# Kernel tuning notes

Measured on AMD Instinct MI355X. Metric: run time of the kernel, lower is better.

Reference implementation:

```python
import jax, jax.numpy as jnp
import numpy as np

N, F, B = 16384, 512, 4
H = 4          # attn heads
MR = 2         # mlp_ratio
GH = max(F // 4, 32)   # gate hidden = 128
SE = F // 8    # SE bottleneck
FH = 512       # fusion_hidden
E = 3          # num experts
EPS = 1e-5


def setup_inputs() -> dict:
    key = jax.random.key(0)
    ks = jax.random.split(key, 24)
    p = lambda k, s: 0.02 * jax.random.normal(k, s, dtype=jnp.float32)
    return {
        'branches': jax.random.normal(ks[0], (N, F, B), dtype=jnp.float32),
        'conv_pw_w': p(ks[1], (F, F)),          # Conv1d k=1, no bias
        'conv_dw_w': p(ks[2], (F, 3)),          # depthwise k=3
        'gn_w': jnp.ones((F,), jnp.float32), 'gn_b': jnp.zeros((F,), jnp.float32),
        'se_w1': p(ks[3], (SE, F)), 'se_w2': p(ks[4], (F, SE)),
        'ln_attn_w': jnp.ones((F,), jnp.float32), 'ln_attn_b': jnp.zeros((F,), jnp.float32),
        'in_proj_w': p(ks[5], (3 * F, F)), 'in_proj_b': jnp.zeros((3 * F,), jnp.float32),
        'attn_out_w': p(ks[6], (F, F)), 'attn_out_b': jnp.zeros((F,), jnp.float32),
        'ln_ffn_w': jnp.ones((F,), jnp.float32), 'ln_ffn_b': jnp.zeros((F,), jnp.float32),
        'ffn_w1': p(ks[7], (MR * F, F)), 'ffn_b1': jnp.zeros((MR * F,), jnp.float32),
        'ffn_w2': p(ks[8], (F, MR * F)), 'ffn_b2': jnp.zeros((F,), jnp.float32),
        'mlp_ln_w': jnp.ones((F,), jnp.float32), 'mlp_ln_b': jnp.zeros((F,), jnp.float32),
        'mlp_w1': p(ks[9], (MR * F, F)), 'mlp_b1': jnp.zeros((MR * F,), jnp.float32),
        'mlp_w2': p(ks[10], (F, MR * F)), 'mlp_b2': jnp.zeros((F,), jnp.float32),
        'gate_w1': p(ks[11], (GH, 2 * F)), 'gate_b1': jnp.zeros((GH,), jnp.float32),
        'gate_w2': p(ks[12], (E, GH)), 'gate_b2': jnp.zeros((E,), jnp.float32),
        'outp_w': p(ks[13], (FH, F)),
    }


def _ln(x, w, b):
    m = jnp.mean(x, -1, keepdims=True)
    v = jnp.mean((x - m) ** 2, -1, keepdims=True)
    return (x - m) * jax.lax.rsqrt(v + EPS) * w + b


def _gelu(x):
    return jax.nn.gelu(x, approximate=False)


def _forward(branches, conv_pw_w, conv_dw_w, gn_w, gn_b, se_w1, se_w2,
             ln_attn_w, ln_attn_b, in_proj_w, in_proj_b, attn_out_w, attn_out_b,
             ln_ffn_w, ln_ffn_b, ffn_w1, ffn_b1, ffn_w2, ffn_b2,
             mlp_ln_w, mlp_ln_b, mlp_w1, mlp_b1, mlp_w2, mlp_b2,
             gate_w1, gate_b1, gate_w2, gate_b2, outp_w):
    # ---- Conv expert ----
    x1 = jnp.einsum('fg,ngb->nfb', conv_pw_w, branches)          # pointwise conv
    xp = jnp.pad(x1, ((0, 0), (0, 0), (1, 1)))                    # depthwise k=3, pad=1
    w0, w1, w2 = (conv_dw_w[:, k][None, :, None] for k in range(3))
    x1 = w0 * xp[:, :, :-2] + w1 * xp[:, :, 1:-1] + w2 * xp[:, :, 2:]
    s = jnp.mean(x1, -1)                                          # SE squeeze (N,F)
    s = jax.nn.sigmoid(jax.nn.relu(s @ se_w1.T) @ se_w2.T)
    x1 = x1 * s[:, :, None]
    m = jnp.mean(x1, (1, 2), keepdims=True)                       # GroupNorm(1 group)
    v = jnp.mean((x1 - m) ** 2, (1, 2), keepdims=True)
    x1 = (x1 - m) * jax.lax.rsqrt(v + EPS) * gn_w[None, :, None] + gn_b[None, :, None]
    x1 = _gelu(x1)
    # ---- Attention expert (branches as tokens) ----
    t = jnp.swapaxes(branches, 1, 2)                              # (N,B,F)
    h = _ln(t, ln_attn_w, ln_attn_b)
    qkv = h @ in_proj_w.T + in_proj_b
    q, k, vv = jnp.split(qkv, 3, axis=-1)
    dh = F // H
    q = q.reshape(N, B, H, dh) * (dh ** -0.5)
    k = k.reshape(N, B, H, dh)
    vv = vv.reshape(N, B, H, dh)
    att = jax.nn.softmax(jnp.einsum('nqhd,nkhd->nhqk', q, k), axis=-1)
    ao = jnp.einsum('nhqk,nkhd->nqhd', att, vv).reshape(N, B, F)
    t = t + ao @ attn_out_w.T + attn_out_b
    h = _ln(t, ln_ffn_w, ln_ffn_b)
    t = t + _gelu(h @ ffn_w1.T + ffn_b1) @ ffn_w2.T + ffn_b2
    x2 = jnp.swapaxes(t, 1, 2)
    # ---- MLP expert ----
    t3 = jnp.swapaxes(branches, 1, 2)
    h3 = _ln(t3, mlp_ln_w, mlp_ln_b)
    t3 = t3 + _gelu(h3 @ mlp_w1.T + mlp_b1) @ mlp_w2.T + mlp_b2
    x3 = jnp.swapaxes(t3, 1, 2)
    # ---- Gating ----
    ctx = jnp.concatenate([jnp.mean(branches, -1), jnp.max(branches, -1)], axis=-1)
    logits = _gelu(ctx @ gate_w1.T + gate_b1) @ gate_w2.T + gate_b2
    alpha = jax.nn.softmax(logits, axis=-1)                       # (N,3)
    fused = (alpha[:, 0, None, None] * x1 + alpha[:, 1, None, None] * x2
             + alpha[:, 2, None, None] * x3)
    return jnp.einsum('of,nfb->nob', outp_w, fused)               # out_proj k=1 conv


def reference(branches, conv_pw_w, conv_dw_w, gn_w, gn_b, se_w1, se_w2,
              ln_attn_w, ln_attn_b, in_proj_w, in_proj_b, attn_out_w, attn_out_b,
              ln_ffn_w, ln_ffn_b, ffn_w1, ffn_b1, ffn_w2, ffn_b2,
              mlp_ln_w, mlp_ln_b, mlp_w1, mlp_b1, mlp_w2, mlp_b2,
              gate_w1, gate_b1, gate_w2, gate_b2, outp_w):
    return _forward(branches, conv_pw_w, conv_dw_w, gn_w, gn_b, se_w1, se_w2,
                    ln_attn_w, ln_attn_b, in_proj_w, in_proj_b, attn_out_w, attn_out_b,
                    ln_ffn_w, ln_ffn_b, ffn_w1, ffn_b1, ffn_w2, ffn_b2,
                    mlp_ln_w, mlp_ln_b, mlp_w1, mlp_b1, mlp_w2, mlp_b2,
                    gate_w1, gate_b1, gate_w2, gate_b2, outp_w)
```

## Files before the change

kernel.cpp:

```cpp
#include <hip/hip_runtime.h>
#include <math.h>


#define N_TOT 16384
#define EPSV 1e-5f

typedef unsigned short u16;
typedef unsigned int   u32;
typedef __attribute__((ext_vector_type(8))) short  short8;
typedef __attribute__((ext_vector_type(4))) float  floatx4;

__device__ __forceinline__ float gelu_exact(float x) {
    return 0.5f * x * (1.0f + erff(x * 0.70710678118654752440f));
}
__device__ __forceinline__ float wave_sum(float v) {
    #pragma unroll
    for (int o = 32; o > 0; o >>= 1) v += __shfl_xor(v, o);
    return v;
}
__device__ __forceinline__ u16 f2bf(float f) {
    u32 u = __float_as_uint(f);
    return (u16)((u + 0x7fffu + ((u >> 16) & 1u)) >> 16);
}
__device__ __forceinline__ u32 pack2(float lo, float hi) {
    return (u32)f2bf(lo) | ((u32)f2bf(hi) << 16);
}
__device__ __forceinline__ float bf1f(u16 u) { return __uint_as_float((u32)u << 16); }
__device__ __forceinline__ float2 bf2f2(u32 u) {
    return make_float2(__uint_as_float(u << 16), __uint_as_float(u & 0xffff0000u));
}
__device__ __forceinline__ void gload_lds16(const void* g, void* l) {
    __builtin_amdgcn_global_load_lds(
        (const __attribute__((address_space(1))) unsigned int*)g,
        (__attribute__((address_space(3))) unsigned int*)l, 16, 0, 0);
}

#define BARR() asm volatile("s_barrier" ::: "memory")
#define VMW(N) asm volatile("s_waitcnt vmcnt(" #N ")" ::: "memory")

#define W_CONVPW 0
#define W_INPROJ 262144
#define W_ATTNO  1048576
#define W_FFN1   1310720
#define W_FFN2   1835008
#define W_MLP1   2359296
#define W_MLP2   2883584
#define W_GATE1  3407872
#define W_SE1    3538944
#define W_SE2    3571712
#define W_OUTP   3604480
#define W_TOT    3866624

__global__ __launch_bounds__(256) void k_w2b(
        const float* __restrict__ p0, const float* __restrict__ p1,
        const float* __restrict__ p2, const float* __restrict__ p3,
        const float* __restrict__ p4, const float* __restrict__ p5,
        const float* __restrict__ p6, const float* __restrict__ p7,
        const float* __restrict__ p8, const float* __restrict__ p9,
        const float* __restrict__ p10, u16* __restrict__ dst)
{
    int i = blockIdx.x * 256 + threadIdx.x;
    if (i >= W_TOT) return;
    const float* s; int off;
    if      (i < W_INPROJ) { s = p0;  off = W_CONVPW; }
    else if (i < W_ATTNO)  { s = p1;  off = W_INPROJ; }
    else if (i < W_FFN1)   { s = p2;  off = W_ATTNO; }
    else if (i < W_FFN2)   { s = p3;  off = W_FFN1; }
    else if (i < W_MLP1)   { s = p4;  off = W_FFN2; }
    else if (i < W_MLP2)   { s = p5;  off = W_MLP1; }
    else if (i < W_GATE1)  { s = p6;  off = W_MLP2; }
    else if (i < W_SE1)    { s = p7;  off = W_GATE1; }
    else if (i < W_SE2)    { s = p8;  off = W_SE1; }
    else if (i < W_OUTP)   { s = p9;  off = W_SE2; }
    else                   { s = p10; off = W_OUTP; }
    dst[i] = f2bf(s[i - off]);
}

__global__ __launch_bounds__(256) void k_prep_ln(const float* __restrict__ br,
        int baseN, u16* __restrict__ Tb, u16* __restrict__ CTX,
        const float* __restrict__ law, const float* __restrict__ lab, u16* __restrict__ LNA,
        const float* __restrict__ lmw, const float* __restrict__ lmb, u16* __restrict__ LNM)
{
    __shared__ float lds[4][4][516];
    int t = threadIdx.x;
    int s0 = blockIdx.x * 4;
    #pragma unroll
    for (int s = 0; s < 4; ++s) {
        const float* p = br + (size_t)(baseN + s0 + s) * 2048;
        u16* c = CTX + (size_t)(s0 + s) * 1024;
        #pragma unroll
        for (int i = 0; i < 2; ++i) {
            int f = t + i * 256;
            float4 v = *(const float4*)(p + f * 4);
            lds[s][0][f] = v.x; lds[s][1][f] = v.y; lds[s][2][f] = v.z; lds[s][3][f] = v.w;
            c[f]       = f2bf((v.x + v.y + v.z + v.w) * 0.25f);
            c[512 + f] = f2bf(fmaxf(fmaxf(v.x, v.y), fmaxf(v.z, v.w)));
        }
    }
    __syncthreads();
    int wv = t >> 6, lane = t & 63, f0 = lane * 8;
    #pragma unroll
    for (int p4i = 0; p4i < 4; ++p4i) {
        int idx = wv * 4 + p4i;
        int s = idx >> 2, b = idx & 3;
        float xv[8];
        #pragma unroll
        for (int i = 0; i < 8; ++i) xv[i] = lds[s][b][f0 + i];
        float sm = 0.f;
        #pragma unroll
        for (int i = 0; i < 8; ++i) sm += xv[i];
        sm = wave_sum(sm);
        float m = sm * (1.f / 512.f);
        float q = 0.f;
        #pragma unroll
        for (int i = 0; i < 8; ++i) { float d = xv[i] - m; q += d * d; }
        q = wave_sum(q);
        float rs = rsqrtf(q * (1.f / 512.f) + EPSV);
        size_t row = (size_t)(s0 + s) * 4 + b;
        *(uint4*)(Tb + row * 512 + f0) = make_uint4(pack2(xv[0], xv[1]), pack2(xv[2], xv[3]),
                                                    pack2(xv[4], xv[5]), pack2(xv[6], xv[7]));
        float o[8];
        #pragma unroll
        for (int i = 0; i < 8; ++i) o[i] = (xv[i] - m) * rs * law[f0 + i] + lab[f0 + i];
        *(uint4*)(LNA + row * 512 + f0) = make_uint4(pack2(o[0], o[1]), pack2(o[2], o[3]),
                                                     pack2(o[4], o[5]), pack2(o[6], o[7]));
        #pragma unroll
        for (int i = 0; i < 8; ++i) o[i] = (xv[i] - m) * rs * lmw[f0 + i] + lmb[f0 + i];
        *(uint4*)(LNM + row * 512 + f0) = make_uint4(pack2(o[0], o[1]), pack2(o[2], o[3]),
                                                     pack2(o[4], o[5]), pack2(o[6], o[7]));
    }
}

__global__ __launch_bounds__(256) void k_ln_b(const u16* __restrict__ X,
        const float* __restrict__ w, const float* __restrict__ b, u16* __restrict__ O)
{
    int t = threadIdx.x;
    int wave = t >> 6, lane = t & 63;
    size_t r = (size_t)blockIdx.x * 4 + wave;
    int f0 = lane * 8;
    uint4 raw = *(const uint4*)(X + r * 512 + f0);
    float xv[8];
    { float2 a = bf2f2(raw.x); xv[0] = a.x; xv[1] = a.y; }
    { float2 a = bf2f2(raw.y); xv[2] = a.x; xv[3] = a.y; }
    { float2 a = bf2f2(raw.z); xv[4] = a.x; xv[5] = a.y; }
    { float2 a = bf2f2(raw.w); xv[6] = a.x; xv[7] = a.y; }
    float s = 0.f;
    #pragma unroll
    for (int i = 0; i < 8; ++i) s += xv[i];
    s = wave_sum(s);
    float m = s * (1.f / 512.f);
    float q = 0.f;
    #pragma unroll
    for (int i = 0; i < 8; ++i) { float d = xv[i] - m; q += d * d; }
    q = wave_sum(q);
    float rs = rsqrtf(q * (1.f / 512.f) + EPSV);
    float o[8];
    #pragma unroll
    for (int i = 0; i < 8; ++i) o[i] = (xv[i] - m) * rs * w[f0 + i] + b[f0 + i];
    *(uint4*)(O + r * 512 + f0) = make_uint4(pack2(o[0], o[1]), pack2(o[2], o[3]),
                                             pack2(o[4], o[5]), pack2(o[6], o[7]));
}


#define STAGE(SLOT, TILE) do {                                                \
    const u16* sm_ = ((SLOT) < 2) ? A : W;                                    \
    int rb_ = (((SLOT) < 2) ? m0 : n0) + ((SLOT) & 1) * 128;                  \
    int k0_ = (TILE) * 64;                                                    \
    u16* db_ = lds + (((TILE) & 1) * 32768) + (SLOT) * 8192;                  \
    _Pragma("unroll")                                                         \
    for (int l_ = 0; l_ < 2; ++l_) {                                          \
        int L_ = (l_ * 512 + tid) * 16;                                       \
        int row_ = L_ >> 7;                                                   \
        int ir_ = (L_ & 127) ^ ((row_ & 7) << 4);                             \
        gload_lds16(sm_ + (size_t)(rb_ + row_) * K + k0_ + (ir_ >> 1),        \
                    db_ + (L_ >> 1));                                         \
    } } while (0)

#define QUAD(MH, NH, STAGESTMT) do {                                          \
    const u16* lb_ = lds + cur * 32768;                                       \
    short8 a_[4][2], b_[2][2];                                                \
    _Pragma("unroll")                                                         \
    for (int mi = 0; mi < 4; ++mi)                                            \
        _Pragma("unroll")                                                     \
        for (int ks = 0; ks < 2; ++ks)                                        \
            a_[mi][ks] = *(const short8*)(lb_ + (MH) * 8192 + arow[mi] + gcol[ks]); \
    _Pragma("unroll")                                                         \
    for (int ni = 0; ni < 2; ++ni)                                            \
        _Pragma("unroll")                                                     \
        for (int ks = 0; ks < 2; ++ks)                                        \
            b_[ni][ks] = *(const short8*)(lb_ + 16384 + (NH) * 8192 + brow[ni] + gcol[ks]); \
    STAGESTMT;                                                                \
    BARR();                                                                   \
    __builtin_amdgcn_s_setprio(1);                                            \
    _Pragma("unroll")                                                         \
    for (int ks = 0; ks < 2; ++ks)                                            \
        _Pragma("unroll")                                                     \
        for (int mi = 0; mi < 4; ++mi)                                        \
            _Pragma("unroll")                                                 \
            for (int ni = 0; ni < 2; ++ni)                                    \
                acc[MH][NH][mi][ni] = __builtin_amdgcn_mfma_f32_16x16x32_bf16( \
                    a_[mi][ks], b_[ni][ks], acc[MH][NH][mi][ni], 0, 0, 0);    \
    __builtin_amdgcn_s_setprio(0);                                            \
} while (0)

template<int EPI, bool HAS_BIAS, bool HAS_RES, int STORE>
__global__ __launch_bounds__(512, 2) void k_gemm256(
        const u16* __restrict__ A, const u16* __restrict__ W,
        const float* __restrict__ bias, const u16* __restrict__ Res,
        void* __restrict__ Cout, int Ncols, int K, int baseN, int nTX,
        const float* __restrict__ dwp, u16* __restrict__ Sout)
{
    __shared__ __align__(16) u16 lds[65536];
    const int tid = threadIdx.x;
    const int wid = tid >> 6, lane = tid & 63;
    const int lr = lane & 15, kg = lane >> 4;
    const int wm = (wid >> 2) * 64;
    const int wn = (wid & 3) * 32;

    int nwg = gridDim.x, orig = blockIdx.x;
    int q = nwg >> 3, r = nwg & 7;
    int xcd = orig & 7, lin = orig >> 3;
    int wgid = (xcd < r ? xcd * (q + 1) : r * (q + 1) + (xcd - r) * q) + lin;
    const int m0 = (wgid / nTX) * 256, n0 = (wgid % nTX) * 256;

    int arow[4], brow[2], gcol[2];
    #pragma unroll
    for (int mi = 0; mi < 4; ++mi) arow[mi] = (wm + mi * 16 + lr) * 64;
    #pragma unroll
    for (int ni = 0; ni < 2; ++ni) brow[ni] = (wn + ni * 16 + lr) * 64;
    #pragma unroll
    for (int ks = 0; ks < 2; ++ks) gcol[ks] = (ks * 32 + kg * 8) ^ ((lr & 7) << 3);

    floatx4 acc[2][2][4][2] = {};

    STAGE(0, 0); STAGE(2, 0); STAGE(1, 0); STAGE(3, 0);

    const int NT = K >> 6;
    int cur = 0;
    for (int t = 0; t < NT - 1; ++t) {
        int nx = t + 1;
        VMW(4); BARR(); QUAD(0, 0, STAGE(0, nx));
        VMW(4); BARR(); QUAD(1, 0, STAGE(2, nx));
        VMW(4); BARR(); QUAD(0, 1, STAGE(1, nx));
                BARR(); QUAD(1, 1, STAGE(3, nx));
        cur ^= 1;
    }
    VMW(4); BARR(); QUAD(0, 0, (void)0);
    VMW(2); BARR(); QUAD(1, 0, (void)0);
    VMW(0); BARR(); QUAD(0, 1, (void)0);
            BARR(); QUAD(1, 1, (void)0);

    int rm = kg * 4;
    #pragma unroll
    for (int MH = 0; MH < 2; ++MH)
    #pragma unroll
    for (int NH = 0; NH < 2; ++NH)
    #pragma unroll
    for (int ni = 0; ni < 2; ++ni) {
        int n = n0 + NH * 128 + wn + ni * 16 + lr;
        float bv = HAS_BIAS ? bias[n] : 0.f;
        float w0, w1, w2;
        if (STORE == 3) { w0 = dwp[n * 3]; w1 = dwp[n * 3 + 1]; w2 = dwp[n * 3 + 2]; }
        #pragma unroll
        for (int mi = 0; mi < 4; ++mi) {
            int mb = m0 + MH * 128 + wm + mi * 16 + rm;
            float vv[4];
            #pragma unroll
            for (int rr = 0; rr < 4; ++rr) {
                float v = acc[MH][NH][mi][ni][rr] + bv;
                if (EPI == 1) v = gelu_exact(v);
                else if (EPI == 2) v = fmaxf(v, 0.f);
                else if (EPI == 3) v = 1.f / (1.f + expf(-v));
                vv[rr] = v;
            }
            if (STORE == 2) {
                *(float4*)((float*)Cout + (size_t)(baseN + (mb >> 2)) * 2048 + (size_t)n * 4)
                    = make_float4(vv[0], vv[1], vv[2], vv[3]);
            } else if (STORE == 3) {
                float y0 = w1 * vv[0] + w2 * vv[1];
                float y1 = w0 * vv[0] + w1 * vv[1] + w2 * vv[2];
                float y2 = w0 * vv[1] + w1 * vv[2] + w2 * vv[3];
                float y3 = w0 * vv[2] + w1 * vv[3];
                u16* xp = (u16*)Cout + (size_t)mb * Ncols + n;
                xp[0] = f2bf(y0);
                xp[Ncols] = f2bf(y1);
                xp[2 * Ncols] = f2bf(y2);
                xp[3 * Ncols] = f2bf(y3);
                Sout[(size_t)(mb >> 2) * Ncols + n] = f2bf((y0 + y1 + y2 + y3) * 0.25f);
            } else {
                #pragma unroll
                for (int rr = 0; rr < 4; ++rr) {
                    float v = vv[rr];
                    if (HAS_RES) v += bf1f(Res[(size_t)(mb + rr) * Ncols + n]);
                    ((u16*)Cout)[(size_t)(mb + rr) * Ncols + n] = f2bf(v);
                }
            }
        }
    }
}

template<int EPI, bool HAS_BIAS, bool HAS_RES, int STORE>
__global__ __launch_bounds__(256) void k_mfma_gemm(
        const u16* __restrict__ A, const u16* __restrict__ W,
        const float* __restrict__ bias, const u16* __restrict__ Res,
        void* __restrict__ Cout, int M, int Ncols, int K, int baseN)
{
    __shared__ u16 As[128 * 32];
    __shared__ u16 Bs[128 * 32];
    int t = threadIdx.x;
    int wid = t >> 6, lane = t & 63;
    int wm = (wid >> 1) * 64, wn = (wid & 1) * 64;
    int m0 = blockIdx.y * 128, n0 = blockIdx.x * 128;
    int srow = t >> 2;
    int scol = (((t & 3) ^ ((srow >> 1) & 3)) * 8);
    int aR0 = min(m0 + srow, M - 1),      aR1 = min(m0 + 64 + srow, M - 1);
    int bR0 = min(n0 + srow, Ncols - 1),  bR1 = min(n0 + 64 + srow, Ncols - 1);
    const u16* Ap0 = A + (size_t)aR0 * K + scol;
    const u16* Ap1 = A + (size_t)aR1 * K + scol;
    const u16* Wp0 = W + (size_t)bR0 * K + scol;
    const u16* Wp1 = W + (size_t)bR1 * K + scol;
    u16* AsT0 = As + t * 8;  u16* AsT1 = As + 2048 + t * 8;
    u16* BsT0 = Bs + t * 8;  u16* BsT1 = Bs + 2048 + t * 8;

    int kg = lane >> 4, lr = lane & 15;
    int cb = kg ^ ((lr >> 1) & 3);
    const u16* aF = As + (wm + lr) * 32 + cb * 8;
    const u16* bF = Bs + (wn + lr) * 32 + cb * 8;

    floatx4 acc[4][4] = {};
    for (int k0 = 0; k0 < K; k0 += 32) {
        __syncthreads();
        gload_lds16(Ap0 + k0, AsT0);
        gload_lds16(Ap1 + k0, AsT1);
        gload_lds16(Wp0 + k0, BsT0);
        gload_lds16(Wp1 + k0, BsT1);
        __syncthreads();
        short8 a[4], b[4];
        #pragma unroll
        for (int i = 0; i < 4; ++i) {
            a[i] = *(const short8*)(aF + i * 512);
            b[i] = *(const short8*)(bF + i * 512);
        }
        #pragma unroll
        for (int i = 0; i < 4; ++i)
            #pragma unroll
            for (int j = 0; j < 4; ++j)
                acc[i][j] = __builtin_amdgcn_mfma_f32_16x16x32_bf16(a[i], b[j], acc[i][j], 0, 0, 0);
    }
    int rm = (lane >> 4) * 4;
    #pragma unroll
    for (int j = 0; j < 4; ++j) {
        int n = n0 + wn + j * 16 + lr;
        float bv = HAS_BIAS ? bias[min(n, Ncols - 1)] : 0.f;
        #pragma unroll
        for (int i = 0; i < 4; ++i) {
            int mb = m0 + wm + i * 16 + rm;
            float vv[4];
            #pragma unroll
            for (int r = 0; r < 4; ++r) {
                float v = acc[i][j][r] + bv;
                if (EPI == 1) v = gelu_exact(v);
                else if (EPI == 2) v = fmaxf(v, 0.f);
                else if (EPI == 3) v = 1.f / (1.f + expf(-v));
                vv[r] = v;
            }
            #pragma unroll
            for (int r = 0; r < 4; ++r) {
                int m = mb + r;
                if (m < M && n < Ncols) {
                    float v = vv[r];
                    if (HAS_RES) v += bf1f(Res[(size_t)m * Ncols + n]);
                    if (STORE == 0) ((float*)Cout)[(size_t)m * Ncols + n] = v;
                    else            ((u16*)Cout)[(size_t)m * Ncols + n] = f2bf(v);
                }
            }
        }
    }
// ... 66 lines not shown
        float dx = xr[b].x - m, dy = xr[b].y - m;
        q += dx * dx + dy * dy;
    }
    q = wave_sum(q);
    if (lane == 0) red[4 + wave] = q;
    __syncthreads();
    float rs = rsqrtf((red[4] + red[5] + red[6] + red[7]) * (1.f / 2048.f) + EPSV);
    const float* a = alpha + (size_t)(baseN + ls) * 3;
    float a0 = a[0], a1 = a[1], a2 = a[2];
    float gw0 = gnw[f], gw1 = gnw[f + 1], gb0 = gnb[f], gb1 = gnb[f + 1];
    #pragma unroll
    for (int b = 0; b < 4; ++b) {
        float x1a = gelu_exact((xr[b].x - m) * rs * gw0 + gb0);
        float x1b = gelu_exact((xr[b].y - m) * rs * gw1 + gb1);
        float2 v2 = bf2f2(*(const u32*)(X2 + (ls * 4 + b) * 512 + f));
        float2 v3 = bf2f2(*(const u32*)(X3 + (ls * 4 + b) * 512 + f));
        *(u32*)(FU + (ls * 4 + b) * 512 + f) =
            pack2(a0 * x1a + a1 * v2.x + a2 * v3.x,
                  a0 * x1b + a1 * v2.y + a2 * v3.y);
    }
}

__global__ __launch_bounds__(256) void k_gate2(const u16* __restrict__ G1,
        const float* __restrict__ w2, const float* __restrict__ b2,
        float* __restrict__ alpha, int CH)
{
    int s = blockIdx.x * 256 + threadIdx.x;
    if (s >= CH) return;
    float l0 = b2[0], l1 = b2[1], l2 = b2[2];
    const u16* g = G1 + (size_t)s * 128;
    for (int j = 0; j < 128; j += 2) {
        float2 gg = bf2f2(*(const u32*)(g + j));
        l0 += gg.x * w2[j]       + gg.y * w2[j + 1];
        l1 += gg.x * w2[128 + j] + gg.y * w2[129 + j];
        l2 += gg.x * w2[256 + j] + gg.y * w2[257 + j];
    }
    float mx = fmaxf(l0, fmaxf(l1, l2));
    float e0 = expf(l0 - mx), e1 = expf(l1 - mx), e2 = expf(l2 - mx);
    float inv = 1.f / (e0 + e1 + e2);
    float* a = alpha + (size_t)s * 3;
    a[0] = e0 * inv; a[1] = e1 * inv; a[2] = e2 * inv;
}

extern "C" void kernel_launch(void* const* d_in, const int* in_sizes, int n_in,
                              void* d_out, int out_size, void* d_ws, size_t ws_size,
                              hipStream_t stream)
{
    (void)in_sizes; (void)n_in; (void)out_size;
    const float* br         = (const float*)d_in[0];
    const float* conv_pw_w  = (const float*)d_in[1];
    const float* conv_dw_w  = (const float*)d_in[2];
    const float* gn_w       = (const float*)d_in[3];
    const float* gn_b       = (const float*)d_in[4];
    const float* se_w1      = (const float*)d_in[5];
    const float* se_w2      = (const float*)d_in[6];
    const float* ln_attn_w  = (const float*)d_in[7];
    const float* ln_attn_b  = (const float*)d_in[8];
    const float* in_proj_w  = (const float*)d_in[9];
    const float* in_proj_b  = (const float*)d_in[10];
    const float* attn_out_w = (const float*)d_in[11];
    const float* attn_out_b = (const float*)d_in[12];
    const float* ln_ffn_w   = (const float*)d_in[13];
    const float* ln_ffn_b   = (const float*)d_in[14];
    const float* ffn_w1     = (const float*)d_in[15];
    const float* ffn_b1     = (const float*)d_in[16];
    const float* ffn_w2     = (const float*)d_in[17];
    const float* ffn_b2     = (const float*)d_in[18];
    const float* mlp_ln_w   = (const float*)d_in[19];
    const float* mlp_ln_b   = (const float*)d_in[20];
    const float* mlp_w1     = (const float*)d_in[21];
    const float* mlp_b1     = (const float*)d_in[22];
    const float* mlp_w2     = (const float*)d_in[23];
    const float* mlp_b2     = (const float*)d_in[24];
    const float* gate_w1    = (const float*)d_in[25];
    const float* gate_b1    = (const float*)d_in[26];
    const float* gate_w2    = (const float*)d_in[27];
    const float* gate_b2    = (const float*)d_in[28];
    const float* outp_w     = (const float*)d_in[29];
    float* out = (float*)d_out;

    char* ws = (char*)d_ws;
    float* alpha = (float*)ws;
    u16* Wb = (u16*)(ws + 196608);
    const size_t CB = 196608 + (size_t)W_TOT * 2;
    int CH = N_TOT;
    while (CH > 64 && CB + (size_t)CH * 31104ULL > ws_size) CH >>= 1;

    char* p = ws + CB;
    u16* Tb   = (u16*)p; p += (size_t)CH * 4096;
    char* CTXS = p;      p += (size_t)CH * 2048;
    u16* LNA  = (u16*)p; p += (size_t)CH * 4096;
    u16* LNM  = (u16*)p; p += (size_t)CH * 4096;
    u16* QKV  = (u16*)p; p += (size_t)CH * 12288;
    u16* AOXP = (u16*)p; p += (size_t)CH * 4096;
    u16* H1   = (u16*)p; p += (size_t)CH * 128;
    u16* G1   = (u16*)p; p += (size_t)CH * 256;
    u16* CTX  = (u16*)CTXS;
    u16* S    = (u16*)CTXS;
    u16* SIGb = (u16*)(CTXS + (size_t)CH * 1024);
    u16* U    = QKV;
    u16* LNF  = LNA;
    u16* FU   = LNM;

    u16* O16 = (u16*)d_out;

    k_w2b<<<(W_TOT + 255) / 256, 256, 0, stream>>>(
        conv_pw_w, in_proj_w, attn_out_w, ffn_w1, ffn_w2, mlp_w1, mlp_w2,
        gate_w1, se_w1, se_w2, outp_w, Wb);

    const int Ri = CH * 4;
    auto g128 = [](int M, int Nc) { return dim3((Nc + 127) / 128, (M + 127) / 128); };
    auto g256 = [](int M, int Nc) { return dim3((M / 256) * (Nc / 256)); };

    for (int c0 = 0; c0 < N_TOT; c0 += CH) {
        u16* X2b  = O16 + (size_t)c0 * 2048;
        u16* T2X3 = O16 + (size_t)N_TOT * 2048 + (size_t)c0 * 2048;

        k_prep_ln<<<CH / 4, 256, 0, stream>>>(br, c0, Tb, CTX,
                                              ln_attn_w, ln_attn_b, LNA,
                                              mlp_ln_w, mlp_ln_b, LNM);
        k_mfma_gemm<1, true, false, 1><<<g128(CH, 128), 256, 0, stream>>>(
            CTX, Wb + W_GATE1, gate_b1, nullptr, G1, CH, 128, 1024, 0);
        k_gate2<<<(CH + 255) / 256, 256, 0, stream>>>(G1, gate_w2, gate_b2,
                                                      alpha + (size_t)c0 * 3, CH);
        k_gemm256<0, true, false, 1><<<g256(Ri, 1536), 512, 0, stream>>>(
            LNA, Wb + W_INPROJ, in_proj_b, nullptr, QKV, 1536, 512, 0, 6, nullptr, nullptr);
        k_attn<<<CH, 256, 0, stream>>>(QKV, AOXP);
        k_gemm256<0, true, true, 1><<<g256(Ri, 512), 512, 0, stream>>>(
            AOXP, Wb + W_ATTNO, attn_out_b, Tb, T2X3, 512, 512, 0, 2, nullptr, nullptr);
        k_ln_b<<<Ri / 4, 256, 0, stream>>>(T2X3, ln_ffn_w, ln_ffn_b, LNF);
        k_gemm256<1, true, false, 1><<<g256(Ri, 1024), 512, 0, stream>>>(
            LNF, Wb + W_FFN1, ffn_b1, nullptr, U, 1024, 512, 0, 4, nullptr, nullptr);
        k_gemm256<0, true, true, 1><<<g256(Ri, 512), 512, 0, stream>>>(
            U, Wb + W_FFN2, ffn_b2, T2X3, X2b, 512, 1024, 0, 2, nullptr, nullptr);
        k_gemm256<1, true, false, 1><<<g256(Ri, 1024), 512, 0, stream>>>(
            LNM, Wb + W_MLP1, mlp_b1, nullptr, U, 1024, 512, 0, 4, nullptr, nullptr);
        k_gemm256<0, true, true, 1><<<g256(Ri, 512), 512, 0, stream>>>(
            U, Wb + W_MLP2, mlp_b2, Tb, T2X3, 512, 1024, 0, 2, nullptr, nullptr);
        k_gemm256<0, false, false, 3><<<g256(Ri, 512), 512, 0, stream>>>(
            Tb, Wb + W_CONVPW, nullptr, nullptr, AOXP, 512, 512, 0, 2, conv_dw_w, S);
        k_mfma_gemm<2, false, false, 1><<<g128(CH, 64), 256, 0, stream>>>(
            S, Wb + W_SE1, nullptr, nullptr, H1, CH, 64, 512, 0);
        k_mfma_gemm<3, false, false, 1><<<g128(CH, 512), 256, 0, stream>>>(
            H1, Wb + W_SE2, nullptr, nullptr, SIGb, CH, 512, 64, 0);
        k_gnfin_fuse<<<CH, 256, 0, stream>>>(AOXP, SIGb, gn_w, gn_b,
                                             X2b, T2X3, alpha, c0, FU);
        k_gemm256<0, false, false, 2><<<g256(Ri, 512), 512, 0, stream>>>(
            FU, Wb + W_OUTP, nullptr, nullptr, out, 512, 512, c0, 2, nullptr, nullptr);
    }
}
```

Measured before the change: 1.036 ms.

## Stage bf16 GEMM epilogue through swizzled LDS for coalesced 16-byte stores

For the plain bf16-store GEMM variant, the MFMA operands are swapped so each lane holds four consecutive output columns. Bias and residual can then be loaded as vectors, and results are packed into an XOR-swizzled LDS tile. The whole 256x256 tile is then written to global memory with coalesced 16-byte stores, replacing scattered 2-byte per-element stores and residual loads. This adds an extra barrier and an LDS round trip at the end of each tile.

After: 1.163 ms. 12.2% more time.

```diff
diff --git a/kernel.cpp b/kernel.cpp
--- a/kernel.cpp
+++ b/kernel.cpp
@@ -34,9 +34,15 @@
         (const __attribute__((address_space(1))) unsigned int*)g,
         (__attribute__((address_space(3))) unsigned int*)l, 16, 0, 0);
 }
+template<bool S>
+__device__ __forceinline__ floatx4 mfma_do(short8 a, short8 b, floatx4 c) {
+    if (S) return __builtin_amdgcn_mfma_f32_16x16x32_bf16(b, a, c, 0, 0, 0);
+    else   return __builtin_amdgcn_mfma_f32_16x16x32_bf16(a, b, c, 0, 0, 0);
+}
 
 #define BARR() asm volatile("s_barrier" ::: "memory")
 #define VMW(N) asm volatile("s_waitcnt vmcnt(" #N ")" ::: "memory")
+#define LGKM0() asm volatile("s_waitcnt lgkmcnt(0)" ::: "memory")
 
 #define W_CONVPW 0
 #define W_INPROJ 262144
@@ -198,8 +204,8 @@
         for (int mi = 0; mi < 4; ++mi)                                        \
             _Pragma("unroll")                                                 \
             for (int ni = 0; ni < 2; ++ni)                                    \
-                acc[MH][NH][mi][ni] = __builtin_amdgcn_mfma_f32_16x16x32_bf16( \
-                    a_[mi][ks], b_[ni][ks], acc[MH][NH][mi][ni], 0, 0, 0);    \
+                acc[MH][NH][mi][ni] = mfma_do<SWAPD>(                         \
+                    a_[mi][ks], b_[ni][ks], acc[MH][NH][mi][ni]);             \
     __builtin_amdgcn_s_setprio(0);                                            \
 } while (0)
 
@@ -210,6 +216,7 @@
         void* __restrict__ Cout, int Ncols, int K, int baseN, int nTX,
         const float* __restrict__ dwp, u16* __restrict__ Sout)
 {
+    constexpr bool SWAPD = (STORE == 1);
     __shared__ __align__(16) u16 lds[65536];
     const int tid = threadIdx.x;
     const int wid = tid >> 6, lane = tid & 63;
@@ -250,49 +257,85 @@
     VMW(0); BARR(); QUAD(0, 1, (void)0);
             BARR(); QUAD(1, 1, (void)0);
 
-    int rm = kg * 4;
-    #pragma unroll
-    for (int MH = 0; MH < 2; ++MH)
-    #pragma unroll
-    for (int NH = 0; NH < 2; ++NH)
-    #pragma unroll
-    for (int ni = 0; ni < 2; ++ni) {
-        int n = n0 + NH * 128 + wn + ni * 16 + lr;
-        float bv = HAS_BIAS ? bias[n] : 0.f;
-        float w0, w1, w2;
-        if (STORE == 3) { w0 = dwp[n * 3]; w1 = dwp[n * 3 + 1]; w2 = dwp[n * 3 + 2]; }
-        #pragma unroll
-        for (int mi = 0; mi < 4; ++mi) {
-            int mb = m0 + MH * 128 + wm + mi * 16 + rm;
-            float vv[4];
+    if (STORE == 1) {
+        BARR();
+        #pragma unroll
+        for (int MH = 0; MH < 2; ++MH)
+        #pragma unroll
+        for (int NH = 0; NH < 2; ++NH)
+        #pragma unroll
+        for (int ni = 0; ni < 2; ++ni) {
+            int nl = NH * 128 + wn + ni * 16 + kg * 4;
+            float4 bv4 = HAS_BIAS ? *(const float4*)(bias + n0 + nl)
+                                  : make_float4(0.f, 0.f, 0.f, 0.f);
             #pragma unroll
-            for (int rr = 0; rr < 4; ++rr) {
-                float v = acc[MH][NH][mi][ni][rr] + bv;
-                if (EPI == 1) v = gelu_exact(v);
-                else if (EPI == 2) v = fmaxf(v, 0.f);
-                else if (EPI == 3) v = 1.f / (1.f + expf(-v));
-                vv[rr] = v;
-            }
-            if (STORE == 2) {
-                *(float4*)((float*)Cout + (size_t)(baseN + (mb >> 2)) * 2048 + (size_t)n * 4)
-                    = make_float4(vv[0], vv[1], vv[2], vv[3]);
-            } else if (STORE == 3) {
-                float y0 = w1 * vv[0] + w2 * vv[1];
-                float y1 = w0 * vv[0] + w1 * vv[1] + w2 * vv[2];
-                float y2 = w0 * vv[1] + w1 * vv[2] + w2 * vv[3];
-                float y3 = w0 * vv[2] + w1 * vv[3];
-                u16* xp = (u16*)Cout + (size_t)mb * Ncols + n;
-                xp[0] = f2bf(y0);
-                xp[Ncols] = f2bf(y1);
-                xp[2 * Ncols] = f2bf(y2);
-                xp[3 * Ncols] = f2bf(y3);
-                Sout[(size_t)(mb >> 2) * Ncols + n] = f2bf((y0 + y1 + y2 + y3) * 0.25f);
-            } else {
+            for (int mi = 0; mi < 4; ++mi) {
+                int ml = MH * 128 + wm + mi * 16 + lr;
+                float v[4];
                 #pragma unroll
                 for (int rr = 0; rr < 4; ++rr) {
-                    float v = vv[rr];
-                    if (HAS_RES) v += bf1f(Res[(size_t)(mb + rr) * Ncols + n]);
-                    ((u16*)Cout)[(size_t)(mb + rr) * Ncols + n] = f2bf(v);
+                    float x = acc[MH][NH][mi][ni][rr] + (&bv4.x)[rr];
+                    if (EPI == 1) x = gelu_exact(x);
+                    else if (EPI == 2) x = fmaxf(x, 0.f);
+                    else if (EPI == 3) x = 1.f / (1.f + expf(-x));
+                    v[rr] = x;
+                }
+                if (HAS_RES) {
+                    uint2 r8 = *(const uint2*)(Res + (size_t)(m0 + ml) * Ncols + n0 + nl);
+                    float2 ra = bf2f2(r8.x), rb = bf2f2(r8.y);
+                    v[0] += ra.x; v[1] += ra.y; v[2] += rb.x; v[3] += rb.y;
+                }
+                int byte = ml * 512 + ((nl * 2) ^ ((ml & 7) << 4));
+                *(uint2*)((char*)lds + byte) = make_uint2(pack2(v[0], v[1]), pack2(v[2], v[3]));
+            }
+        }
+        LGKM0();
+        BARR();
+        #pragma unroll
+        for (int i = 0; i < 16; ++i) {
+            int L = tid * 256 + i * 16;
+            int ml = L >> 9, off = L & 511;
+            uint4 d = *(const uint4*)((const char*)lds + ml * 512 + (off ^ ((ml & 7) << 4)));
+            *(uint4*)((u16*)Cout + (size_t)(m0 + ml) * Ncols + n0 + (off >> 1)) = d;
+        }
+    } else {
+        int rm = kg * 4;
+        #pragma unroll
+        for (int MH = 0; MH < 2; ++MH)
+        #pragma unroll
+        for (int NH = 0; NH < 2; ++NH)
+        #pragma unroll
+        for (int ni = 0; ni < 2; ++ni) {
+            int n = n0 + NH * 128 + wn + ni * 16 + lr;
+            float bv = HAS_BIAS ? bias[n] : 0.f;
+            float w0, w1, w2;
+            if (STORE == 3) { w0 = dwp[n * 3]; w1 = dwp[n * 3 + 1]; w2 = dwp[n * 3 + 2]; }
+            #pragma unroll
+            for (int mi = 0; mi < 4; ++mi) {
+                int mb = m0 + MH * 128 + wm + mi * 16 + rm;
+                float vv[4];
+                #pragma unroll
+                for (int rr = 0; rr < 4; ++rr) {
+                    float v = acc[MH][NH][mi][ni][rr] + bv;
+                    if (EPI == 1) v = gelu_exact(v);
+                    else if (EPI == 2) v = fmaxf(v, 0.f);
+                    else if (EPI == 3) v = 1.f / (1.f + expf(-v));
+                    vv[rr] = v;
+                }
+                if (STORE == 2) {
+                    *(float4*)((float*)Cout + (size_t)(baseN + (mb >> 2)) * 2048 + (size_t)n * 4)
+                        = make_float4(vv[0], vv[1], vv[2], vv[3]);
+                } else if (STORE == 3) {
+                    float y0 = w1 * vv[0] + w2 * vv[1];
+                    float y1 = w0 * vv[0] + w1 * vv[1] + w2 * vv[2];
+                    float y2 = w0 * vv[1] + w1 * vv[2] + w2 * vv[3];
+                    float y3 = w0 * vv[2] + w1 * vv[3];
+                    u16* xp = (u16*)Cout + (size_t)mb * Ncols + n;
+                    xp[0] = f2bf(y0);
+                    xp[Ncols] = f2bf(y1);
+                    xp[2 * Ncols] = f2bf(y2);
+                    xp[3 * Ncols] = f2bf(y3);
+                    Sout[(size_t)(mb >> 2) * Ncols + n] = f2bf((y0 + y1 + y2 + y3) * 0.25f);
                 }
             }
         }
```

## Restructure bf16 GEMM mainloop to 4-slot K=32 pipeline with larger per-wave tiles

Applied to the files above, without the earlier changes.

The 256x256 GEMM mainloop now uses K tiles of 32 instead of 64, held in a 4-slot LDS ring with three tiles in flight, replacing the two-buffer quadrant schedule. Each wave now owns a 128x64 output region (8x4 MFMA accumulators) rather than four 64x32 quadrants. Each tile is computed in two MFMA half-steps, with the A and B staging loads for a later tile issued between them. The aim is deeper load/compute overlap and more fragment reuse per LDS read. In exchange there are more barriers per K element and the same accumulator register count under the 512x2 launch bounds.

Result: slower. 1.349 ms (+30.2%).

```diff
diff --git a/kernel.cpp b/kernel.cpp
--- a/kernel.cpp
+++ b/kernel.cpp
@@ -162,44 +162,58 @@
 }
 
 
-#define STAGE(SLOT, TILE) do {                                                \
-    const u16* sm_ = ((SLOT) < 2) ? A : W;                                    \
-    int rb_ = (((SLOT) < 2) ? m0 : n0) + ((SLOT) & 1) * 128;                  \
-    int k0_ = (TILE) * 64;                                                    \
-    u16* db_ = lds + (((TILE) & 1) * 32768) + (SLOT) * 8192;                  \
+#define STG_A(TILE) do {                                                      \
+    int sl_ = (TILE) & 3;                                                     \
     _Pragma("unroll")                                                         \
     for (int l_ = 0; l_ < 2; ++l_) {                                          \
-        int L_ = (l_ * 512 + tid) * 16;                                       \
-        int row_ = L_ >> 7;                                                   \
-        int ir_ = (L_ & 127) ^ ((row_ & 7) << 4);                             \
-        gload_lds16(sm_ + (size_t)(rb_ + row_) * K + k0_ + (ir_ >> 1),        \
-                    db_ + (L_ >> 1));                                         \
+        int E_ = (l_ * 512 + tid) * 8;                                        \
+        int r_ = E_ >> 6, c_ = E_ & 63;                                       \
+        int cp_ = c_ ^ ((r_ & 7) << 3);                                       \
+        gload_lds16(A + (size_t)(m0 + r_ + ((cp_ >> 5) << 7)) * K             \
+                        + (TILE) * 32 + (cp_ & 31),                           \
+                    lds + sl_ * 16384 + E_);                                  \
     } } while (0)
 
-#define QUAD(MH, NH, STAGESTMT) do {                                          \
-    const u16* lb_ = lds + cur * 32768;                                       \
-    short8 a_[4][2], b_[2][2];                                                \
+#define STG_B(TILE) do {                                                      \
+    int sl_ = (TILE) & 3;                                                     \
+    _Pragma("unroll")                                                         \
+    for (int l_ = 0; l_ < 2; ++l_) {                                          \
+        int E_ = (l_ * 512 + tid) * 8;                                        \
+        int r_ = E_ >> 6, c_ = E_ & 63;                                       \
+        int cp_ = c_ ^ ((r_ & 7) << 3);                                       \
+        gload_lds16(W + (size_t)(n0 + r_ + ((cp_ >> 5) << 7)) * K             \
+                        + (TILE) * 32 + (cp_ & 31),                           \
+                    lds + sl_ * 16384 + 8192 + E_);                           \
+    } } while (0)
+
+#define TILE_BODY(S, SA, SB) do {                                             \
+    const u16* lb_ = lds + (S) * 16384;                                       \
+    short8 a_[4], b_[4];                                                      \
+    _Pragma("unroll")                                                         \
+    for (int ni = 0; ni < 4; ++ni) b_[ni] = *(const short8*)(lb_ + 8192 + boff[ni]); \
+    _Pragma("unroll")                                                         \
+    for (int mi = 0; mi < 4; ++mi) a_[mi] = *(const short8*)(lb_ + aoff[mi]); \
+    SA;                                                                       \
+    BARR();                                                                   \
+    __builtin_amdgcn_s_setprio(1);                                            \
     _Pragma("unroll")                                                         \
     for (int mi = 0; mi < 4; ++mi)                                            \
         _Pragma("unroll")                                                     \
-        for (int ks = 0; ks < 2; ++ks)                                        \
-            a_[mi][ks] = *(const short8*)(lb_ + (MH) * 8192 + arow[mi] + gcol[ks]); \
+        for (int ni = 0; ni < 4; ++ni)                                        \
+            acc[mi][ni] = __builtin_amdgcn_mfma_f32_16x16x32_bf16(            \
+                a_[mi], b_[ni], acc[mi][ni], 0, 0, 0);                        \
+    __builtin_amdgcn_s_setprio(0);                                            \
     _Pragma("unroll")                                                         \
-    for (int ni = 0; ni < 2; ++ni)                                            \
-        _Pragma("unroll")                                                     \
-        for (int ks = 0; ks < 2; ++ks)                                        \
-            b_[ni][ks] = *(const short8*)(lb_ + 16384 + (NH) * 8192 + brow[ni] + gcol[ks]); \
-    STAGESTMT;                                                                \
+    for (int mi = 0; mi < 4; ++mi) a_[mi] = *(const short8*)(lb_ + aoff[4 + mi]); \
+    SB;                                                                       \
     BARR();                                                                   \
     __builtin_amdgcn_s_setprio(1);                                            \
     _Pragma("unroll")                                                         \
-    for (int ks = 0; ks < 2; ++ks)                                            \
+    for (int mi = 0; mi < 4; ++mi)                                            \
         _Pragma("unroll")                                                     \
-        for (int mi = 0; mi < 4; ++mi)                                        \
-            _Pragma("unroll")                                                 \
-            for (int ni = 0; ni < 2; ++ni)                                    \
-                acc[MH][NH][mi][ni] = __builtin_amdgcn_mfma_f32_16x16x32_bf16( \
-                    a_[mi][ks], b_[ni][ks], acc[MH][NH][mi][ni], 0, 0, 0);    \
+        for (int ni = 0; ni < 4; ++ni)                                        \
+            acc[4 + mi][ni] = __builtin_amdgcn_mfma_f32_16x16x32_bf16(        \
+                a_[mi], b_[ni], acc[4 + mi][ni], 0, 0, 0);                    \
     __builtin_amdgcn_s_setprio(0);                                            \
 } while (0)
 
@@ -214,8 +228,8 @@
     const int tid = threadIdx.x;
     const int wid = tid >> 6, lane = tid & 63;
     const int lr = lane & 15, kg = lane >> 4;
-    const int wm = (wid >> 2) * 64;
-    const int wn = (wid & 3) * 32;
+    const int wm = (wid >> 2) * 128;
+    const int wn = (wid & 3) * 64;
 
     int nwg = gridDim.x, orig = blockIdx.x;
     int q = nwg >> 3, r = nwg & 7;
@@ -223,51 +237,48 @@
     int wgid = (xcd < r ? xcd * (q + 1) : r * (q + 1) + (xcd - r) * q) + lin;
     const int m0 = (wgid / nTX) * 256, n0 = (wgid % nTX) * 256;
 
-    int arow[4], brow[2], gcol[2];
-    #pragma unroll
-    for (int mi = 0; mi < 4; ++mi) arow[mi] = (wm + mi * 16 + lr) * 64;
-    #pragma unroll
-    for (int ni = 0; ni < 2; ++ni) brow[ni] = (wn + ni * 16 + lr) * 64;
-    #pragma unroll
-    for (int ks = 0; ks < 2; ++ks) gcol[ks] = (ks * 32 + kg * 8) ^ ((lr & 7) << 3);
-
-    floatx4 acc[2][2][4][2] = {};
-
-    STAGE(0, 0); STAGE(2, 0); STAGE(1, 0); STAGE(3, 0);
-
-    const int NT = K >> 6;
-    int cur = 0;
-    for (int t = 0; t < NT - 1; ++t) {
-        int nx = t + 1;
-        VMW(4); BARR(); QUAD(0, 0, STAGE(0, nx));
-        VMW(4); BARR(); QUAD(1, 0, STAGE(2, nx));
-        VMW(4); BARR(); QUAD(0, 1, STAGE(1, nx));
-                BARR(); QUAD(1, 1, STAGE(3, nx));
-        cur ^= 1;
-    }
-    VMW(4); BARR(); QUAD(0, 0, (void)0);
-    VMW(2); BARR(); QUAD(1, 0, (void)0);
-    VMW(0); BARR(); QUAD(0, 1, (void)0);
-            BARR(); QUAD(1, 1, (void)0);
-
-    int rm = kg * 4;
-    #pragma unroll
-    for (int MH = 0; MH < 2; ++MH)
-    #pragma unroll
-    for (int NH = 0; NH < 2; ++NH)
-    #pragma unroll
-    for (int ni = 0; ni < 2; ++ni) {
-        int n = n0 + NH * 128 + wn + ni * 16 + lr;
+    int aoff[8], boff[4];
+    #pragma unroll
+    for (int mi = 0; mi < 8; ++mi) {
+        int R = wm + mi * 16 + lr;
+        int rr_ = R & 127;
+        aoff[mi] = rr_ * 64 + ((((R >> 7) << 5) + kg * 8) ^ ((rr_ & 7) << 3));
+    }
+    #pragma unroll
+    for (int ni = 0; ni < 4; ++ni) {
+        int R = wn + ni * 16 + lr;
+        int rr_ = R & 127;
+        boff[ni] = rr_ * 64 + ((((R >> 7) << 5) + kg * 8) ^ ((rr_ & 7) << 3));
+    }
+
+    floatx4 acc[8][4] = {};
+
+    STG_A(0); STG_B(0);
+    STG_A(1); STG_B(1);
+    STG_A(2); STG_B(2);
+
+    const int NT = K >> 5;
+    for (int t = 0; t < NT - 3; ++t) {
+        VMW(8); BARR();
+        TILE_BODY(t & 3, STG_A(t + 3), STG_B(t + 3));
+    }
+    VMW(8); BARR(); TILE_BODY((NT - 3) & 3, (void)0, (void)0);
+    VMW(4); BARR(); TILE_BODY((NT - 2) & 3, (void)0, (void)0);
+    VMW(0); BARR(); TILE_BODY((NT - 1) & 3, (void)0, (void)0);
+
+    #pragma unroll
+    for (int ni = 0; ni < 4; ++ni) {
+        int n = n0 + wn + ni * 16 + lr;
         float bv = HAS_BIAS ? bias[n] : 0.f;
         float w0, w1, w2;
         if (STORE == 3) { w0 = dwp[n * 3]; w1 = dwp[n * 3 + 1]; w2 = dwp[n * 3 + 2]; }
         #pragma unroll
-        for (int mi = 0; mi < 4; ++mi) {
-            int mb = m0 + MH * 128 + wm + mi * 16 + rm;
+        for (int mi = 0; mi < 8; ++mi) {
+            int mb = m0 + wm + mi * 16 + kg * 4;
             float vv[4];
             #pragma unroll
             for (int rr = 0; rr < 4; ++rr) {
-                float v = acc[MH][NH][mi][ni][rr] + bv;
+                float v = acc[mi][ni][rr] + bv;
                 if (EPI == 1) v = gelu_exact(v);
                 else if (EPI == 2) v = fmaxf(v, 0.f);
                 else if (EPI == 3) v = 1.f / (1.f + expf(-v));
```

## Fold LayerNorm affine into following GEMM weights and epilogue

Applied to the files above, without the earlier changes.

Folds the LayerNorm weight into the in_proj, ffn1 and mlp1 weight rows, and precomputes per-column sums and bias constants once per call. The GEMMs then read the raw bf16 activations and apply per-row mean/rstd in the epilogue. This removes writing and reading the normalized LNA, LNM and LNF tensors and turns the ffn LayerNorm kernel into a stats-only pass. The cost is more epilogue work per element and a numerical change, since the mean is now subtracted after a bf16 GEMM on uncentered inputs.

Result: slower. 1.057 ms (+2.0%).

```diff
diff --git a/kernel.cpp b/kernel.cpp
--- a/kernel.cpp
+++ b/kernel.cpp
@@ -76,10 +76,50 @@
     dst[i] = f2bf(s[i - off]);
 }
 
+__global__ __launch_bounds__(256) void k_wfold(
+        const float* __restrict__ wA, const float* __restrict__ lnwA,
+        const float* __restrict__ lnbA, const float* __restrict__ biasA,
+        const float* __restrict__ wF, const float* __restrict__ lnwF,
+        const float* __restrict__ lnbF, const float* __restrict__ biasF,
+        const float* __restrict__ wM, const float* __restrict__ lnwM,
+        const float* __restrict__ lnbM, const float* __restrict__ biasM,
+        u16* __restrict__ Wb,
+        float* __restrict__ sA, float* __restrict__ cA,
+        float* __restrict__ sF, float* __restrict__ cF,
+        float* __restrict__ sM, float* __restrict__ cM)
+{
+    __shared__ float rs_[4], rc_[4];
+    int r = blockIdx.x, t = threadIdx.x;
+    const float *W, *lnw, *lnb, *bias;
+    u16* dst; float *sp, *cp; int row;
+    if (r < 1536)      { W = wA; lnw = lnwA; lnb = lnbA; bias = biasA;
+                         dst = Wb + W_INPROJ; sp = sA; cp = cA; row = r; }
+    else if (r < 2560) { W = wF; lnw = lnwF; lnb = lnbF; bias = biasF;
+                         dst = Wb + W_FFN1;   sp = sF; cp = cF; row = r - 1536; }
+    else               { W = wM; lnw = lnwM; lnb = lnbM; bias = biasM;
+                         dst = Wb + W_MLP1;   sp = sM; cp = cM; row = r - 2560; }
+    const float* wr = W + (size_t)row * 512;
+    float s = 0.f, c = 0.f;
+    #pragma unroll
+    for (int i = 0; i < 2; ++i) {
+        int k = t + i * 256;
+        float wv = lnw[k] * wr[k];
+        dst[(size_t)row * 512 + k] = f2bf(wv);
+        s += wv;
+        c += lnb[k] * wr[k];
+    }
+    s = wave_sum(s); c = wave_sum(c);
+    if ((t & 63) == 0) { rs_[t >> 6] = s; rc_[t >> 6] = c; }
+    __syncthreads();
+    if (t == 0) {
+        sp[row] = rs_[0] + rs_[1] + rs_[2] + rs_[3];
+        cp[row] = rc_[0] + rc_[1] + rc_[2] + rc_[3] + bias[row];
+    }
+}
+
 __global__ __launch_bounds__(256) void k_prep_ln(const float* __restrict__ br,
         int baseN, u16* __restrict__ Tb, u16* __restrict__ CTX,
-        const float* __restrict__ law, const float* __restrict__ lab, u16* __restrict__ LNA,
-        const float* __restrict__ lmw, const float* __restrict__ lmb, u16* __restrict__ LNM)
+        float2* __restrict__ STA)
 {
     __shared__ float lds[4][4][516];
     int t = threadIdx.x;
@@ -119,20 +159,12 @@
         size_t row = (size_t)(s0 + s) * 4 + b;
         *(uint4*)(Tb + row * 512 + f0) = make_uint4(pack2(xv[0], xv[1]), pack2(xv[2], xv[3]),
                                                     pack2(xv[4], xv[5]), pack2(xv[6], xv[7]));
-        float o[8];
-        #pragma unroll
-        for (int i = 0; i < 8; ++i) o[i] = (xv[i] - m) * rs * law[f0 + i] + lab[f0 + i];
-        *(uint4*)(LNA + row * 512 + f0) = make_uint4(pack2(o[0], o[1]), pack2(o[2], o[3]),
-                                                     pack2(o[4], o[5]), pack2(o[6], o[7]));
-        #pragma unroll
-        for (int i = 0; i < 8; ++i) o[i] = (xv[i] - m) * rs * lmw[f0 + i] + lmb[f0 + i];
-        *(uint4*)(LNM + row * 512 + f0) = make_uint4(pack2(o[0], o[1]), pack2(o[2], o[3]),
-                                                     pack2(o[4], o[5]), pack2(o[6], o[7]));
-    }
-}
-
-__global__ __launch_bounds__(256) void k_ln_b(const u16* __restrict__ X,
-        const float* __restrict__ w, const float* __restrict__ b, u16* __restrict__ O)
+        if (lane == 0) STA[row] = make_float2(rs, rs * m);
+    }
+}
+
+__global__ __launch_bounds__(256) void k_lnstats(const u16* __restrict__ X,
+        float2* __restrict__ ST)
 {
     int t = threadIdx.x;
     int wave = t >> 6, lane = t & 63;
@@ -154,11 +186,7 @@
     for (int i = 0; i < 8; ++i) { float d = xv[i] - m; q += d * d; }
     q = wave_sum(q);
     float rs = rsqrtf(q * (1.f / 512.f) + EPSV);
-    float o[8];
-    #pragma unroll
-    for (int i = 0; i < 8; ++i) o[i] = (xv[i] - m) * rs * w[f0 + i] + b[f0 + i];
-    *(uint4*)(O + r * 512 + f0) = make_uint4(pack2(o[0], o[1]), pack2(o[2], o[3]),
-                                             pack2(o[4], o[5]), pack2(o[6], o[7]));
+    if (lane == 0) ST[r] = make_float2(rs, rs * m);
 }
 
 
@@ -203,12 +231,14 @@
     __builtin_amdgcn_s_setprio(0);                                            \
 } while (0)
 
-template<int EPI, bool HAS_BIAS, bool HAS_RES, int STORE>
+template<int EPI, bool HAS_BIAS, bool HAS_RES, int STORE, bool LNFOLD>
 __global__ __launch_bounds__(512, 2) void k_gemm256(
         const u16* __restrict__ A, const u16* __restrict__ W,
         const float* __restrict__ bias, const u16* __restrict__ Res,
         void* __restrict__ Cout, int Ncols, int K, int baseN, int nTX,
-        const float* __restrict__ dwp, u16* __restrict__ Sout)
+        const float* __restrict__ dwp, u16* __restrict__ Sout,
+        const float2* __restrict__ Astat, const float* __restrict__ Scol,
+        const float* __restrict__ Ccol)
 {
     __shared__ __align__(16) u16 lds[65536];
     const int tid = threadIdx.x;
@@ -259,6 +289,8 @@
     for (int ni = 0; ni < 2; ++ni) {
         int n = n0 + NH * 128 + wn + ni * 16 + lr;
         float bv = HAS_BIAS ? bias[n] : 0.f;
+        float s_n = 0.f, c_n = 0.f;
+        if (LNFOLD) { s_n = Scol[n]; c_n = Ccol[n]; }
         float w0, w1, w2;
         if (STORE == 3) { w0 = dwp[n * 3]; w1 = dwp[n * 3 + 1]; w2 = dwp[n * 3 + 2]; }
         #pragma unroll
@@ -267,7 +299,13 @@
             float vv[4];
             #pragma unroll
             for (int rr = 0; rr < 4; ++rr) {
-                float v = acc[MH][NH][mi][ni][rr] + bv;
+                float v;
+                if (LNFOLD) {
+                    float2 st = Astat[mb + rr];
+                    v = acc[MH][NH][mi][ni][rr] * st.x - st.y * s_n + c_n;
+                } else {
+                    v = acc[MH][NH][mi][ni][rr] + bv;
+                }
                 if (EPI == 1) v = gelu_exact(v);
                 else if (EPI == 2) v = fmaxf(v, 0.f);
                 else if (EPI == 3) v = 1.f / (1.f + expf(-v));
@@ -525,31 +563,41 @@
     char* ws = (char*)d_ws;
     float* alpha = (float*)ws;
     u16* Wb = (u16*)(ws + 196608);
-    const size_t CB = 196608 + (size_t)W_TOT * 2;
+    float* sA = (float*)(ws + 196608 + (size_t)W_TOT * 2);
+    float* cA = sA + 1536;
+    float* sF = cA + 1536;
+    float* cF = sF + 1024;
+    float* sM = cF + 1024;
+    float* cM = sM + 1024;
+    const size_t CB = 196608 + (size_t)W_TOT * 2 + 28672;
     int CH = N_TOT;
-    while (CH > 64 && CB + (size_t)CH * 31104ULL > ws_size) CH >>= 1;
+    while (CH > 64 && CB + (size_t)CH * 27072ULL > ws_size) CH >>= 1;
 
     char* p = ws + CB;
-    u16* Tb   = (u16*)p; p += (size_t)CH * 4096;
-    char* CTXS = p;      p += (size_t)CH * 2048;
-    u16* LNA  = (u16*)p; p += (size_t)CH * 4096;
-    u16* LNM  = (u16*)p; p += (size_t)CH * 4096;
-    u16* QKV  = (u16*)p; p += (size_t)CH * 12288;
-    u16* AOXP = (u16*)p; p += (size_t)CH * 4096;
-    u16* H1   = (u16*)p; p += (size_t)CH * 128;
-    u16* G1   = (u16*)p; p += (size_t)CH * 256;
+    u16* Tb    = (u16*)p;    p += (size_t)CH * 4096;
+    char* CTXS = p;          p += (size_t)CH * 2048;
+    u16* FU    = (u16*)p;    p += (size_t)CH * 4096;
+    u16* QKV   = (u16*)p;    p += (size_t)CH * 12288;
+    u16* AOXP  = (u16*)p;    p += (size_t)CH * 4096;
+    u16* H1    = (u16*)p;    p += (size_t)CH * 128;
+    u16* G1    = (u16*)p;    p += (size_t)CH * 256;
+    float2* STA = (float2*)p; p += (size_t)CH * 32;
+    float2* ST2 = (float2*)p; p += (size_t)CH * 32;
     u16* CTX  = (u16*)CTXS;
     u16* S    = (u16*)CTXS;
     u16* SIGb = (u16*)(CTXS + (size_t)CH * 1024);
     u16* U    = QKV;
-    u16* LNF  = LNA;
-    u16* FU   = LNM;
 
     u16* O16 = (u16*)d_out;
 
     k_w2b<<<(W_TOT + 255) / 256, 256, 0, stream>>>(
         conv_pw_w, in_proj_w, attn_out_w, ffn_w1, ffn_w2, mlp_w1, mlp_w2,
         gate_w1, se_w1, se_w2, outp_w, Wb);
+    k_wfold<<<3584, 256, 0, stream>>>(
+        in_proj_w, ln_attn_w, ln_attn_b, in_proj_b,
+        ffn_w1, ln_ffn_w, ln_ffn_b, ffn_b1,
+        mlp_w1, mlp_ln_w, mlp_ln_b, mlp_b1,
+        Wb, sA, cA, sF, cF, sM, cM);
 
     const int Ri = CH * 4;
     auto g128 = [](int M, int Nc) { return dim3((Nc + 127) / 128, (M + 127) / 128); };
@@ -559,36 +607,42 @@
         u16* X2b  = O16 + (size_t)c0 * 2048;
         u16* T2X3 = O16 + (size_t)N_TOT * 2048 + (size_t)c0 * 2048;
 
-        k_prep_ln<<<CH / 4, 256, 0, stream>>>(br, c0, Tb, CTX,
-                                              ln_attn_w, ln_attn_b, LNA,
-                                              mlp_ln_w, mlp_ln_b, LNM);
+        k_prep_ln<<<CH / 4, 256, 0, stream>>>(br, c0, Tb, CTX, STA);
         k_mfma_gemm<1, true, false, 1><<<g128(CH, 128), 256, 0, stream>>>(
             CTX, Wb + W_GATE1, gate_b1, nullptr, G1, CH, 128, 1024, 0);
         k_gate2<<<(CH + 255) / 256, 256, 0, stream>>>(G1, gate_w2, gate_b2,
                                                       alpha + (size_t)c0 * 3, CH);
-        k_gemm256<0, true, false, 1><<<g256(Ri, 1536), 512, 0, stream>>>(
-            LNA, Wb + W_INPROJ, in_proj_b, nullptr, QKV, 1536, 512, 0, 6, nullptr, nullptr);
+        k_gemm256<0, false, false, 1, true><<<g256(Ri, 1536), 512, 0, stream>>>(
+            Tb, Wb + W_INPROJ, nullptr, nullptr, QKV, 1536, 512, 0, 6,
+            nullptr, nullptr, STA, sA, cA);
         k_attn<<<CH, 256, 0, stream>>>(QKV, AOXP);
-        k_gemm256<0, true, true, 1><<<g256(Ri, 512), 512, 0, stream>>>(
-            AOXP, Wb + W_ATTNO, attn_out_b, Tb, T2X3, 512, 512, 0, 2, nullptr, nullptr);
-        k_ln_b<<<Ri / 4, 256, 0, stream>>>(T2X3, ln_ffn_w, ln_ffn_b, LNF);
-        k_gemm256<1, true, false, 1><<<g256(Ri, 1024), 512, 0, stream>>>(
-            LNF, Wb + W_FFN1, ffn_b1, nullptr, U, 1024, 512, 0, 4, nullptr, nullptr);
-        k_gemm256<0, true, true, 1><<<g256(Ri, 512), 512, 0, stream>>>(
-            U, Wb + W_FFN2, ffn_b2, T2X3, X2b, 512, 1024, 0, 2, nullptr, nullptr);
-        k_gemm256<1, true, false, 1><<<g256(Ri, 1024), 512, 0, stream>>>(
-            LNM, Wb + W_MLP1, mlp_b1, nullptr, U, 1024, 512, 0, 4, nullptr, nullptr);
-        k_gemm256<0, true, true, 1><<<g256(Ri, 512), 512, 0, stream>>>(
-            U, Wb + W_MLP2, mlp_b2, Tb, T2X3, 512, 1024, 0, 2, nullptr, nullptr);
-        k_gemm256<0, false, false, 3><<<g256(Ri, 512), 512, 0, stream>>>(
-            Tb, Wb + W_CONVPW, nullptr, nullptr, AOXP, 512, 512, 0, 2, conv_dw_w, S);
+        k_gemm256<0, true, true, 1, false><<<g256(Ri, 512), 512, 0, stream>>>(
+            AOXP, Wb + W_ATTNO, attn_out_b, Tb, T2X3, 512, 512, 0, 2,
+            nullptr, nullptr, nullptr, nullptr, nullptr);
+        k_lnstats<<<Ri / 4, 256, 0, stream>>>(T2X3, ST2);
+        k_gemm256<1, false, false, 1, true><<<g256(Ri, 1024), 512, 0, stream>>>(
+            T2X3, Wb + W_FFN1, nullptr, nullptr, U, 1024, 512, 0, 4,
+            nullptr, nullptr, ST2, sF, cF);
+        k_gemm256<0, true, true, 1, false><<<g256(Ri, 512), 512, 0, stream>>>(
+            U, Wb + W_FFN2, ffn_b2, T2X3, X2b, 512, 1024, 0, 2,
+            nullptr, nullptr, nullptr, nullptr, nullptr);
+        k_gemm256<1, false, false, 1, true><<<g256(Ri, 1024), 512, 0, stream>>>(
+            Tb, Wb + W_MLP1, nullptr, nullptr, U, 1024, 512, 0, 4,
+            nullptr, nullptr, STA, sM, cM);
+        k_gemm256<0, true, true, 1, false><<<g256(Ri, 512), 512, 0, stream>>>(
+            U, Wb + W_MLP2, mlp_b2, Tb, T2X3, 512, 1024, 0, 2,
+            nullptr, nullptr, nullptr, nullptr, nullptr);
+        k_gemm256<0, false, false, 3, false><<<g256(Ri, 512), 512, 0, stream>>>(
+            Tb, Wb + W_CONVPW, nullptr, nullptr, AOXP, 512, 512, 0, 2,
+            conv_dw_w, S, nullptr, nullptr, nullptr);
         k_mfma_gemm<2, false, false, 1><<<g128(CH, 64), 256, 0, stream>>>(
             S, Wb + W_SE1, nullptr, nullptr, H1, CH, 64, 512, 0);
         k_mfma_gemm<3, false, false, 1><<<g128(CH, 512), 256, 0, stream>>>(
             H1, Wb + W_SE2, nullptr, nullptr, SIGb, CH, 512, 64, 0);
         k_gnfin_fuse<<<CH, 256, 0, stream>>>(AOXP, SIGb, gn_w, gn_b,
                                              X2b, T2X3, alpha, c0, FU);
-        k_gemm256<0, false, false, 2><<<g256(Ri, 512), 512, 0, stream>>>(
-            FU, Wb + W_OUTP, nullptr, nullptr, out, 512, 512, c0, 2, nullptr, nullptr);
-    }
-}
+        k_gemm256<0, false, false, 2, false><<<g256(Ri, 512), 512, 0, stream>>>(
+            FU, Wb + W_OUTP, nullptr, nullptr, out, 512, 512, c0, 2,
+            nullptr, nullptr, nullptr, nullptr, nullptr);
+    }
+}
```
